# Kernel tuning notes

Measured on AMD Instinct MI355X. Metric: run time of the kernel, lower is better.

## Reference

```python
import jax, jax.numpy as jnp
import numpy as np

N, E, FN, FE, HID, G, OUT = 50000, 1600000, 16, 8, 64, 8, 1
NEG_ATT = 0.2   # GATv2 attention LeakyReLU slope (PyG default)
NEG_ACT = 0.01  # F.leaky_relu / nn.LeakyReLU default slope
EPS_BN = 1e-5


def _lin(k, fi, fo):
    return jax.random.normal(k, (fi, fo), jnp.float32) / float(np.sqrt(fi))


def setup_inputs() -> dict:
    key = jax.random.key(0)
    ks = iter(jax.random.split(key, 64))
    nk = lambda: next(ks)
    d = {}
    d['x'] = jax.random.normal(nk(), (N, FN), jnp.float32)
    d['edge_index'] = jax.random.randint(nk(), (2, E), 0, N)
    d['edge_attr'] = jax.random.normal(nk(), (E, FE), jnp.float32)
    d['batch'] = jnp.sort(jax.random.randint(nk(), (N,), 0, G))
    d['node_W'] = _lin(nk(), FN, HID); d['node_b'] = jnp.zeros((HID,), jnp.float32)
    d['eemb_W'] = _lin(nk(), FE, HID); d['eemb_b'] = jnp.zeros((HID,), jnp.float32)
    for i, h in enumerate((4, 4, 1)):
        c = HID // h
        d[f'Wl{i}'] = _lin(nk(), HID, HID); d[f'bl{i}'] = jnp.zeros((HID,), jnp.float32)
        d[f'Wr{i}'] = _lin(nk(), HID, HID); d[f'br{i}'] = jnp.zeros((HID,), jnp.float32)
        d[f'Wed{i}'] = _lin(nk(), HID, HID)  # lin_edge has bias=False in PyG
        d[f'att{i}'] = jax.random.normal(nk(), (h, c), jnp.float32) / float(np.sqrt(c))
        d[f'cb{i}'] = jnp.zeros((HID,), jnp.float32)
        d[f'g{i}'] = jnp.ones((HID,), jnp.float32); d[f'bt{i}'] = jnp.zeros((HID,), jnp.float32)
    d['ro1_W'] = _lin(nk(), HID, HID // 2); d['ro1_b'] = jnp.zeros((HID // 2,), jnp.float32)
    d['ro2_W'] = _lin(nk(), HID // 2, OUT); d['ro2_b'] = jnp.zeros((OUT,), jnp.float32)
    return d


def _gatv2(xn, src, dst, ea, Wl, bl, Wr, br, Wed, att, cb):
    # PyG GATv2Conv (concat=True, share_weights=False), self-loops already in src/dst/ea.
    n = xn.shape[0]
    h, c = att.shape
    xl = (xn @ Wl + bl).reshape(n, h, c)   # source transform (messages)
    xr = (xn @ Wr + br).reshape(n, h, c)   # destination transform
    e = (ea @ Wed).reshape(-1, h, c)       # edge transform
    m = jax.nn.leaky_relu(xl[src] + xr[dst] + e, NEG_ATT)  # [Etot,h,c]
    alpha = jnp.einsum('ehc,hc->eh', m, att)               # [Etot,h]
    amax = jax.lax.stop_gradient(jax.ops.segment_max(alpha, dst, num_segments=n))
    ex = jnp.exp(alpha - amax[dst])
    den = jax.ops.segment_sum(ex, dst, num_segments=n)
    a = ex / den[dst]                                      # segment softmax over in-edges
    out = jax.ops.segment_sum(a[:, :, None] * xl[src], dst, num_segments=n)
    return out.reshape(n, h * c) + cb


def _bn(x, g, b):
    # BatchNorm with batch statistics (training-mode normalization)
    mu = x.mean(0)
    var = x.var(0)
    return (x - mu) * jax.lax.rsqrt(var + EPS_BN) * g + b


def _forward(x, edge_index, edge_attr, batch, node_W, node_b, eemb_W, eemb_b,
             Wl0, bl0, Wr0, br0, Wed0, att0, cb0, g0, bt0,
             Wl1, bl1, Wr1, br1, Wed1, att1, cb1, g1, bt1,
             Wl2, bl2, Wr2, br2, Wed2, att2, cb2, g2, bt2,
             ro1_W, ro1_b, ro2_W, ro2_b):
    n = x.shape[0]
    loop = jnp.arange(n)
    src = jnp.concatenate([edge_index[0], loop])  # add self loops (PyG default)
    dst = jnp.concatenate([edge_index[1], loop])
    ea = jax.nn.leaky_relu(edge_attr @ eemb_W + eemb_b, NEG_ACT)  # edge_emb
    ea = jnp.concatenate([ea, jnp.broadcast_to(ea.mean(0), (n, HID))], 0)  # fill_value='mean'
    xh = x @ node_W + node_b
    layers = ((Wl0, bl0, Wr0, br0, Wed0, att0, cb0, g0, bt0),
              (Wl1, bl1, Wr1, br1, Wed1, att1, cb1, g1, bt1),
              (Wl2, bl2, Wr2, br2, Wed2, att2, cb2, g2, bt2))
    for (Wl, bl, Wr, br, Wed, att, cb, g, b) in layers:
        xh = _gatv2(xh, src, dst, ea, Wl, bl, Wr, br, Wed, att, cb)
        xh = jax.nn.leaky_relu(_bn(xh, g, b), NEG_ACT)
    pooled = jax.ops.segment_sum(xh, batch, num_segments=G)  # global_add_pool
    hidr = jax.nn.leaky_relu(pooled @ ro1_W + ro1_b, NEG_ACT)
    return hidr @ ro2_W + ro2_b


def reference(x, edge_index, edge_attr, batch, node_W, node_b, eemb_W, eemb_b,
              Wl0, bl0, Wr0, br0, Wed0, att0, cb0, g0, bt0,
              Wl1, bl1, Wr1, br1, Wed1, att1, cb1, g1, bt1,
              Wl2, bl2, Wr2, br2, Wed2, att2, cb2, g2, bt2,
              ro1_W, ro1_b, ro2_W, ro2_b):
    return _forward(x, edge_index, edge_attr, batch, node_W, node_b, eemb_W, eemb_b,
                    Wl0, bl0, Wr0, br0, Wed0, att0, cb0, g0, bt0,
                    Wl1, bl1, Wr1, br1, Wed1, att1, cb1, g1, bt1,
                    Wl2, bl2, Wr2, br2, Wed2, att2, cb2, g2, bt2,
                    ro1_W, ro1_b, ro2_W, ro2_b)
```

## Files before the change

### kernel.cpp

```cpp
#include <hip/hip_runtime.h>
#include <stdint.h>

#define N_NODES 50000
#define N_EDGES 1600000
#define ETOT    (N_EDGES + N_NODES)
#define FN 16
#define FE 8
#define HID 64
#define NGR 8
#define NEG_ATT 0.2f
#define NEG_ACT 0.01f
#define EPS_BN 1e-5f
#define MEAN_BLOCKS 512
#define SELF_FLAG 0x40000000
#define SRC_MASK  0x3FFFFFFF
#define SCAN_BLOCKS 196

typedef __attribute__((ext_vector_type(8))) short short8;
typedef __attribute__((ext_vector_type(4))) float f32x4;

__device__ __forceinline__ float bf2f(unsigned short u) {
  union { unsigned int i; float f; } c; c.i = ((unsigned int)u) << 16; return c.f;
}
__device__ __forceinline__ unsigned short f2bf(float f) {
  union { float f; unsigned int i; } c; c.f = f;
  unsigned int r = c.i + 0x7FFFu + ((c.i >> 16) & 1u);
  return (unsigned short)(r >> 16);
}
__device__ __forceinline__ float lrelu(float x, float s) { return x > 0.f ? x : s * x; }

__global__ __launch_bounds__(256) void k_node_embed(
    const float* __restrict__ x, const float* __restrict__ W,
    const float* __restrict__ b, float* __restrict__ xh) {
  __shared__ float sW[FN * HID];
  int t = threadIdx.x;
  for (int i = t; i < FN * HID; i += 256) sW[i] = W[i];
  __syncthreads();
  int j = t & 63;
  int v = blockIdx.x * 4 + (t >> 6);
  const float* xr = x + v * FN;
  float acc = b[j];
#pragma unroll
  for (int k = 0; k < FN; ++k) acc += xr[k] * sW[k * HID + j];
  xh[v * HID + j] = acc;
}

__global__ __launch_bounds__(256) void k_hist(const int* __restrict__ ei,
                                              int* __restrict__ counts) {
  int i = blockIdx.x * blockDim.x + threadIdx.x;
  int stride = gridDim.x * blockDim.x;
  for (; i < N_EDGES; i += stride) atomicAdd(&counts[ei[N_EDGES + i]], 1);
}

__global__ __launch_bounds__(256) void k_scanA(const int* __restrict__ counts,
                                               int* __restrict__ row_ptr,
                                               int* __restrict__ blocksum) {
  __shared__ int s[256];
  int t = threadIdx.x;
  int v = blockIdx.x * 256 + t;
  int val = (v < N_NODES) ? counts[v] + 1 : 0;
  s[t] = val; __syncthreads();
  for (int off = 1; off < 256; off <<= 1) {
    int add = (t >= off) ? s[t - off] : 0;
    __syncthreads();
    s[t] += add;
    __syncthreads();
  }
  if (v < N_NODES) row_ptr[v] = s[t] - val;
  if (t == 255) blocksum[blockIdx.x] = s[255];
}

__global__ __launch_bounds__(256) void k_scanB(const int* __restrict__ blocksum,
                                               int* __restrict__ blockoff,
                                               int* __restrict__ row_ptr) {
  __shared__ int s[256];
  int t = threadIdx.x;
  int val = (t < SCAN_BLOCKS) ? blocksum[t] : 0;
  s[t] = val; __syncthreads();
  for (int off = 1; off < 256; off <<= 1) {
    int add = (t >= off) ? s[t - off] : 0;
    __syncthreads();
    s[t] += add;
    __syncthreads();
  }
  if (t < SCAN_BLOCKS) blockoff[t] = s[t] - val;
  if (t == 255) row_ptr[N_NODES] = s[255];
}

__global__ __launch_bounds__(256) void k_scanC(int* __restrict__ row_ptr,
                                               int* __restrict__ fill,
                                               const int* __restrict__ blockoff) {
  int t = threadIdx.x;
  int v = blockIdx.x * 256 + t;
  if (v < N_NODES) {
    int rp = row_ptr[v] + blockoff[blockIdx.x];
    row_ptr[v] = rp;
    fill[v] = rp;
  }
}

__global__ __launch_bounds__(256) void k_scatter(const int* __restrict__ ei,
                                                 int* __restrict__ fill,
                                                 int2* __restrict__ srcperm) {
  int i = blockIdx.x * blockDim.x + threadIdx.x;
  int stride = gridDim.x * blockDim.x;
  for (; i < ETOT; i += stride) {
    if (i < N_EDGES) {
      int d = ei[N_EDGES + i];
      int pos = atomicAdd(&fill[d], 1);
      srcperm[pos] = make_int2(ei[i], i);
    } else {
      int v = i - N_EDGES;
      int pos = atomicAdd(&fill[v], 1);
      srcperm[pos] = make_int2(v | SELF_FLAG, 0);
    }
  }
}

__global__ __launch_bounds__(256) void k_attr_cvt(const float* __restrict__ eattr,
                                                  unsigned short* __restrict__ attr_bf) {
  int idx = blockIdx.x * 256 + threadIdx.x;
  float4 a = ((const float4*)eattr)[idx];
  unsigned int lo = (unsigned int)f2bf(a.x) | ((unsigned int)f2bf(a.y) << 16);
  unsigned int hi = (unsigned int)f2bf(a.z) | ((unsigned int)f2bf(a.w) << 16);
  ((int2*)attr_bf)[idx] = make_int2((int)lo, (int)hi);
}

__global__ __launch_bounds__(256) void k_meanp(const float* __restrict__ eattr,
                                               const float* __restrict__ eW,
                                               const float* __restrict__ eb,
                                               float* __restrict__ partial) {
  __shared__ float sA[256 * FE];
  __shared__ float sred[256];
  int t = threadIdx.x; int j = t & 63; int w = t >> 6;
  float Wj[8];
#pragma unroll
  for (int k = 0; k < 8; ++k) Wj[k] = eW[k * HID + j];
  float bj = eb[j], msum = 0.f;
  const int TILES = N_EDGES / 256;
  for (int tile = blockIdx.x; tile < TILES; tile += gridDim.x) {
    __syncthreads();
    const float4* src = (const float4*)(eattr + (size_t)tile * 256 * FE);
    ((float4*)sA)[t] = src[t];
    ((float4*)sA)[t + 256] = src[t + 256];
    __syncthreads();
#pragma unroll 8
    for (int e = 0; e < 64; ++e) {
      const float4* ar = (const float4*)(sA + (w * 64 + e) * FE);
      float4 A0 = ar[0], A1 = ar[1];
      float acc = bj + A0.x * Wj[0] + A0.y * Wj[1] + A0.z * Wj[2] + A0.w * Wj[3]
                     + A1.x * Wj[4] + A1.y * Wj[5] + A1.z * Wj[6] + A1.w * Wj[7];
      msum += lrelu(acc, NEG_ACT);
    }
  }
  sred[t] = msum; __syncthreads();
  if (w == 0)
    partial[blockIdx.x * HID + j] = sred[j] + sred[j + 64] + sred[j + 128] + sred[j + 192];
}

__global__ __launch_bounds__(256) void k_mean(const float* __restrict__ partial,
                                              float* __restrict__ mean) {
  __shared__ float sred[256];
  int t = threadIdx.x; int j = t & 63; int w = t >> 6;
  float s = 0.f;
  for (int bk = w; bk < MEAN_BLOCKS; bk += 4) s += partial[bk * HID + j];
  sred[t] = s; __syncthreads();
  if (w == 0)
    mean[j] = (sred[j] + sred[j + 64] + sred[j + 128] + sred[j + 192]) / (float)N_EDGES;
}

__global__ void k_eself(const float* __restrict__ meanv,
                        const float* __restrict__ Wed,
                        float* __restrict__ e_self) {
  int j = threadIdx.x;
  float s = 0.f;
  for (int k = 0; k < HID; ++k) s += meanv[k] * Wed[k * HID + j];
  e_self[j] = s;
}

__global__ __launch_bounds__(256) void k_xlr(const float* __restrict__ xh,
                                             const float* __restrict__ Wl,
                                             const float* __restrict__ bl,
                                             const float* __restrict__ Wr,
                                             const float* __restrict__ br,
                                             unsigned short* __restrict__ xl_bf,
                                             float* __restrict__ xr) {
  __shared__ float sWl[HID * HID], sWr[HID * HID];
  __shared__ float srow[4][HID];
  int t = threadIdx.x;
  for (int i = t; i < HID * HID; i += 256) { sWl[i] = Wl[i]; sWr[i] = Wr[i]; }
  __syncthreads();
  int j = t & 63; int w = t >> 6;
  int v = blockIdx.x * 4 + w;
  srow[w][j] = xh[v * HID + j];
  __syncthreads();
  float accL = bl[j], accR = br[j];
#pragma unroll
  for (int k = 0; k < HID; ++k) {
    float xk = srow[w][k];
    accL += xk * sWl[k * HID + j];
    accR += xk * sWr[k * HID + j];
  }
  xl_bf[v * HID + j] = f2bf(accL);
  xr[v * HID + j] = accR;
}

template <int HW>
__global__ __launch_bounds__(256) void k_attn_f(
    const unsigned short* __restrict__ xl_bf, const float* __restrict__ xr,
    const unsigned short* __restrict__ attr_bf,
    const int2* __restrict__ srcperm, const int* __restrict__ row_ptr,
    const float* __restrict__ eW, const float* __restrict__ eb,
    const float* __restrict__ Wed, const float* __restrict__ e_self,
    const float* __restrict__ att, const float* __restrict__ cb,
    float* __restrict__ xo) {
  __shared__ __align__(16) char smem[9216 + 16896];
  unsigned short* T1   = (unsigned short*)smem;
  unsigned short* sWed = (unsigned short*)(smem + 9216);
  unsigned short* sEw  = (unsigned short*)(smem + 9216 + 8192);
  float*          sEb  = (float*)(smem + 9216 + 8192 + 1024);
  float*          T2   = (float*)(smem + 9216);

  int t = threadIdx.x;
  for (int i = t; i < HID * HID; i += 256) sWed[i] = f2bf(Wed[i]);
  for (int i = t; i < FE * HID; i += 256) sEw[i] = f2bf(eW[i]);
  if (t < HID) sEb[t] = eb[t];
  __syncthreads();

  int lane = t & 63, w = t >> 6, l15 = lane & 15, lg = lane >> 4;

  short8 bW[4][2];
#pragma unroll
  for (int jc = 0; jc < 4; ++jc)
#pragma unroll
    for (int kh = 0; kh < 2; ++kh)
#pragma unroll
      for (int i = 0; i < 8; ++i)
        bW[jc][kh][i] = (short)sWed[(8 * lg + i + 32 * kh) * HID + jc * 16 + l15];
  short8 bE[4] = {};
  if (lg == 0)
#pragma unroll
    for (int jc = 0; jc < 4; ++jc)
#pragma unroll
      for (int i = 0; i < 8; ++i)
        bE[jc][i] = (short)sEw[i * HID + jc * 16 + l15];
  float biasv[4];
#pragma unroll
  for (int jc = 0; jc < 4; ++jc) biasv[jc] = sEb[jc * 16 + l15];
  __syncthreads();

  int v = blockIdx.x * 4 + w;
  if (v >= N_NODES) return;

  float xrv = xr[v * HID + lane];
  float attj = att[lane];
  float esj = e_self[lane];
  float cbj = cb[lane];
  int beg = row_ptr[v], end = row_ptr[v + 1];
  float M = -3.0e38f, S = 0.f, acc = 0.f;

  unsigned short* T1w = T1 + w * 16 * 72;
  float* T2w = T2 + w * 16 * 66;

  for (int base = beg; base < end; base += 16) {
    int cnt = end - base; if (cnt > 16) cnt = 16;
    int eidx = base + l15; if (eidx >= end) eidx = end - 1;
    int2 sp = srcperm[eidx];

    float xls[16];
#pragma unroll
    for (int i = 0; i < 16; ++i) {
      int raw = __builtin_amdgcn_readlane(sp.x, i);
      unsigned srcv = (unsigned)(raw & SRC_MASK);
      xls[i] = bf2f(xl_bf[srcv * 64u + (unsigned)lane]);
    }

    short8 a0 = {};
    if (lg == 0 && !(sp.x & SELF_FLAG))
      a0 = *(const short8*)(attr_bf + (size_t)sp.y * FE);
    f32x4 accE[4];
#pragma unroll
    for (int jc = 0; jc < 4; ++jc) {
      f32x4 z = {};
      accE[jc] = __builtin_amdgcn_mfma_f32_16x16x32_bf16(a0, bE[jc], z, 0, 0, 0);
    }
#pragma unroll
    for (int jc = 0; jc < 4; ++jc)
#pragma unroll
      for (int i = 0; i < 4; ++i)
        T1w[(4 * lg + i) * 72 + jc * 16 + l15] =
            f2bf(lrelu(accE[jc][i] + biasv[jc], NEG_ACT));
    __builtin_amdgcn_wave_barrier();
    asm volatile("s_waitcnt lgkmcnt(0)" ::: "memory");
    __builtin_amdgcn_sched_barrier(0);

    short8 A0 = *(const short8*)&T1w[l15 * 72 + 8 * lg];
    short8 A1 = *(const short8*)&T1w[l15 * 72 + 32 + 8 * lg];
    f32x4 acc2[4];
#pragma unroll
    for (int jc = 0; jc < 4; ++jc) {
      f32x4 z = {};
      acc2[jc] = __builtin_amdgcn_mfma_f32_16x16x32_bf16(A0, bW[jc][0], z, 0, 0, 0);
      acc2[jc] = __builtin_amdgcn_mfma_f32_16x16x32_bf16(A1, bW[jc][1], acc2[jc], 0, 0, 0);
    }
#pragma unroll
    for (int jc = 0; jc < 4; ++jc)
#pragma unroll
      for (int i = 0; i < 4; ++i)
        T2w[(4 * lg + i) * 66 + jc * 16 + l15] = acc2[jc][i];
    __builtin_amdgcn_wave_barrier();
    asm volatile("s_waitcnt lgkmcnt(0)" ::: "memory");
    __builtin_amdgcn_sched_barrier(0);

    float r[16];
#pragma unroll
    for (int i = 0; i < 16; ++i) {
      int raw = __builtin_amdgcn_readlane(sp.x, i);
      float e = (raw & SELF_FLAG) ? esj : T2w[i * 66 + lane];
      float mm = lrelu(xls[i] + xrv + e, NEG_ATT) * attj;
#pragma unroll
      for (int o = 1; o < HW; o <<= 1) mm += __shfl_xor(mm, o, 64);
      r[i] = (i < cnt) ? mm : -3.0e38f;
    }
    float mx = r[0];
#pragma unroll
    for (int i = 1; i < 16; ++i) mx = fmaxf(mx, r[i]);
    float Mn = fmaxf(M, mx);
    float sc = __expf(M - Mn);
    acc *= sc; S *= sc;
#pragma unroll
    for (int i = 0; i < 16; ++i) {
      float wi = __expf(r[i] - Mn);
      S += wi;
      acc += wi * xls[i];
    }
    M = Mn;
    __builtin_amdgcn_wave_barrier();
  }
  xo[v * HID + lane] = acc / S + cbj;
}

__global__ __launch_bounds__(256) void k_bnstats(const float* __restrict__ xo,
                                                 float* __restrict__ bns) {
  __shared__ float s1[256], s2[256];
  int t = threadIdx.x; int j = t & 63; int r = t >> 6;
  float sum = 0.f, sq = 0.f;
  int stride = gridDim.x * 4;
  for (int v = blockIdx.x * 4 + r; v < N_NODES; v += stride) {
    float x = xo[v * HID + j];
    sum += x; sq += x * x;
  }
  s1[t] = sum; s2[t] = sq; __syncthreads();
  if (r == 0) {
    atomicAdd(&bns[j], s1[j] + s1[j + 64] + s1[j + 128] + s1[j + 192]);
    atomicAdd(&bns[64 + j], s2[j] + s2[j + 64] + s2[j + 128] + s2[j + 192]);
  }
}

__global__ __launch_bounds__(256) void k_bnapply(const float* __restrict__ xo,
                                                 const float* __restrict__ bns,
                                                 const float* __restrict__ g,
                                                 const float* __restrict__ b,
                                                 float* __restrict__ xh) {
  int tid = blockIdx.x * 256 + threadIdx.x;
  int j = tid & 63;
  int v = tid >> 6;
  if (v >= N_NODES) return;
  const float invN = 1.f / (float)N_NODES;
  float mu = bns[j] * invN;
  float var = bns[64 + j] * invN - mu * mu;
  var = fmaxf(var, 0.f);
  float y = (xo[v * HID + j] - mu) * rsqrtf(var + EPS_BN) * g[j] + b[j];
  xh[v * HID + j] = lrelu(y, NEG_ACT);
}

__global__ __launch_bounds__(256) void k_pool(const float* __restrict__ xh,
                                              const int* __restrict__ batch,
                                              float* __restrict__ pooled) {
  __shared__ float lacc[4][NGR][HID];
  int t = threadIdx.x; int j = t & 63; int r = t >> 6;
  float a[NGR];
#pragma unroll
  for (int gg = 0; gg < NGR; ++gg) a[gg] = 0.f;
  int stride = gridDim.x * 4;
  for (int v = blockIdx.x * 4 + r; v < N_NODES; v += stride) {
    int g = batch[v];
    float x = xh[v * HID + j];
#pragma unroll
    for (int gg = 0; gg < NGR; ++gg) a[gg] += (g == gg) ? x : 0.f;
  }
#pragma unroll
  for (int gg = 0; gg < NGR; ++gg) lacc[r][gg][j] = a[gg];
  __syncthreads();
  if (r == 0) {
#pragma unroll
    for (int gg = 0; gg < NGR; ++gg)
      atomicAdd(&pooled[gg * HID + j],
                lacc[0][gg][j] + lacc[1][gg][j] + lacc[2][gg][j] + lacc[3][gg][j]);
  }
}

__global__ __launch_bounds__(256) void k_readout(const float* __restrict__ pooled,
                                                 const float* __restrict__ W1,
                                                 const float* __restrict__ b1,
                                                 const float* __restrict__ W2,
                                                 const float* __restrict__ b2,
                                                 float* __restrict__ out) {
  __shared__ float hid[NGR][32];
  int t = threadIdx.x;
  int g = t >> 5, q = t & 31;
  float acc = b1[q];
  for (int k = 0; k < HID; ++k) acc += pooled[g * HID + k] * W1[k * 32 + q];
  hid[g][q] = lrelu(acc, NEG_ACT);
  __syncthreads();
  if (t < NGR) {
    float o = b2[0];
    for (int q2 = 0; q2 < 32; ++q2) o += hid[t][q2] * W2[q2];
    out[t] = o;
  }
}

extern "C" void kernel_launch(void* const* d_in, const int* in_sizes, int n_in,
                              void* d_out, int out_size, void* d_ws, size_t ws_size,
                              hipStream_t stream) {
  (void)in_sizes; (void)n_in; (void)out_size; (void)ws_size;
  const float* x      = (const float*)d_in[0];
  const int*   ei     = (const int*)d_in[1];
  const float* eattr  = (const float*)d_in[2];
  const int*   batch  = (const int*)d_in[3];
  const float* node_W = (const float*)d_in[4];
  const float* node_b = (const float*)d_in[5];
  const float* eemb_W = (const float*)d_in[6];
  const float* eemb_b = (const float*)d_in[7];
  const float* ro1_W  = (const float*)d_in[35];
  const float* ro1_b  = (const float*)d_in[36];
  const float* ro2_W  = (const float*)d_in[37];
  const float* ro2_b  = (const float*)d_in[38];
  float* out = (float*)d_out;

  char* p = (char*)d_ws;
  auto alloc = [&](size_t bytes) {
    char* r = p;
    p += (bytes + 255) & ~(size_t)255;
    return r;
  };
  int*   counts = (int*)alloc((size_t)N_NODES * 4);
  float* bns    = (float*)alloc(3 * 128 * 4);
  float* pooled = (float*)alloc(NGR * HID * 4);
  size_t zero_bytes = (size_t)(p - (char*)d_ws);
  int*   row_ptr  = (int*)alloc((size_t)(N_NODES + 1) * 4);
  int*   fill     = (int*)alloc((size_t)N_NODES * 4);
  int*   blocksum = (int*)alloc((size_t)SCAN_BLOCKS * 4);
  int*   blockoff = (int*)alloc((size_t)SCAN_BLOCKS * 4);
  int2*  srcperm  = (int2*)alloc((size_t)ETOT * 8);
  unsigned short* attr_bf = (unsigned short*)alloc((size_t)N_EDGES * FE * 2);
  float* partial = (float*)alloc((size_t)MEAN_BLOCKS * HID * 4);
  float* meanv   = (float*)alloc(HID * 4);
  float* e_self  = (float*)alloc(HID * 4);
  float* xh      = (float*)alloc((size_t)N_NODES * HID * 4);
  unsigned short* xl_bf = (unsigned short*)alloc((size_t)N_NODES * HID * 2);
  float* xr      = (float*)alloc((size_t)N_NODES * HID * 4);
  float* xo      = xh;

  hipMemsetAsync(d_ws, 0, zero_bytes, stream);

  k_node_embed<<<N_NODES / 4, 256, 0, stream>>>(x, node_W, node_b, xh);
  k_hist<<<1024, 256, 0, stream>>>(ei, counts);
  k_scanA<<<SCAN_BLOCKS, 256, 0, stream>>>(counts, row_ptr, blocksum);
  k_scanB<<<1, 256, 0, stream>>>(blocksum, blockoff, row_ptr);
  k_scanC<<<SCAN_BLOCKS, 256, 0, stream>>>(row_ptr, fill, blockoff);
  k_scatter<<<1024, 256, 0, stream>>>(ei, fill, srcperm);
  k_attr_cvt<<<N_EDGES * FE / 4 / 256, 256, 0, stream>>>(eattr, attr_bf);
  k_meanp<<<MEAN_BLOCKS, 256, 0, stream>>>(eattr, eemb_W, eemb_b, partial);
  k_mean<<<1, 256, 0, stream>>>(partial, meanv);

  const int ablocks = (N_NODES + 3) / 4;
  for (int L = 0; L < 3; ++L) {
    const float* Wl  = (const float*)d_in[8 + 9 * L + 0];
    const float* bl  = (const float*)d_in[8 + 9 * L + 1];
    const float* Wr  = (const float*)d_in[8 + 9 * L + 2];
    const float* br  = (const float*)d_in[8 + 9 * L + 3];
    const float* Wed = (const float*)d_in[8 + 9 * L + 4];
    const float* att = (const float*)d_in[8 + 9 * L + 5];
    const float* cb  = (const float*)d_in[8 + 9 * L + 6];
    const float* g   = (const float*)d_in[8 + 9 * L + 7];
    const float* bt  = (const float*)d_in[8 + 9 * L + 8];
    k_xlr<<<N_NODES / 4, 256, 0, stream>>>(xh, Wl, bl, Wr, br, xl_bf, xr);
    k_eself<<<1, 64, 0, stream>>>(meanv, Wed, e_self);
    if (L < 2)
      k_attn_f<16><<<ablocks, 256, 0, stream>>>(xl_bf, xr, attr_bf, srcperm, row_ptr,
                                                eemb_W, eemb_b, Wed, e_self, att, cb, xo);
    else
      k_attn_f<64><<<ablocks, 256, 0, stream>>>(xl_bf, xr, attr_bf, srcperm, row_ptr,
                                                eemb_W, eemb_b, Wed, e_self, att, cb, xo);
    k_bnstats<<<256, 256, 0, stream>>>(xo, bns + L * 128);
    k_bnapply<<<N_NODES * HID / 256, 256, 0, stream>>>(xo, bns + L * 128, g, bt, xh);
  }

  k_pool<<<64, 256, 0, stream>>>(xh, batch, pooled);
  k_readout<<<1, 256, 0, stream>>>(pooled, ro1_W, ro1_b, ro2_W, ro2_b, out);
}
```

Baseline: 1.629 ms.

## Split fused GATv2 attention into edge-parallel score and node aggregation kernels

The per-node fused attention kernel is replaced by two kernels. An edge-tiled scoring kernel processes fixed 16-edge tiles across the whole CSR edge list: it gathers xl+xr as MFMA accumulators, folds the edge projection and the attention dot product into MFMA ops, and writes per-edge alpha values. A per-node aggregation kernel then does an online softmax over the stored alphas. A precomputed per-edge destination array replaces per-node tiling, which removes the padding waste on ragged neighbour lists and the per-lane shuffle reductions. The costs are an extra alpha buffer written and read per layer, redundant gathers of xl, and edge attributes converted from fp32 on every layer instead of once.

```diff
diff --git a/kernel.cpp b/kernel.cpp
--- a/kernel.cpp
+++ b/kernel.cpp
@@ -117,13 +117,13 @@
   }
 }
 
-__global__ __launch_bounds__(256) void k_attr_cvt(const float* __restrict__ eattr,
-                                                  unsigned short* __restrict__ attr_bf) {
-  int idx = blockIdx.x * 256 + threadIdx.x;
-  float4 a = ((const float4*)eattr)[idx];
-  unsigned int lo = (unsigned int)f2bf(a.x) | ((unsigned int)f2bf(a.y) << 16);
-  unsigned int hi = (unsigned int)f2bf(a.z) | ((unsigned int)f2bf(a.w) << 16);
-  ((int2*)attr_bf)[idx] = make_int2((int)lo, (int)hi);
+__global__ __launch_bounds__(256) void k_filldst(const int* __restrict__ row_ptr,
+                                                 int* __restrict__ dst_s) {
+  int t = threadIdx.x; int lane = t & 63; int w = t >> 6;
+  int v = blockIdx.x * 4 + w;
+  if (v >= N_NODES) return;
+  int beg = row_ptr[v], end = row_ptr[v + 1];
+  for (int p = beg + lane; p < end; p += 64) dst_s[p] = v;
 }
 
 __global__ __launch_bounds__(256) void k_meanp(const float* __restrict__ eattr,
@@ -169,15 +169,6 @@
     mean[j] = (sred[j] + sred[j + 64] + sred[j + 128] + sred[j + 192]) / (float)N_EDGES;
 }
 
-__global__ void k_eself(const float* __restrict__ meanv,
-                        const float* __restrict__ Wed,
-                        float* __restrict__ e_self) {
-  int j = threadIdx.x;
-  float s = 0.f;
-  for (int k = 0; k < HID; ++k) s += meanv[k] * Wed[k * HID + j];
-  e_self[j] = s;
-}
-
 __global__ __launch_bounds__(256) void k_xlr(const float* __restrict__ xh,
                                              const float* __restrict__ Wl,
                                              const float* __restrict__ bl,
@@ -206,25 +197,23 @@
 }
 
 template <int HW>
-__global__ __launch_bounds__(256) void k_attn_f(
+__global__ __launch_bounds__(256) void k_score(
     const unsigned short* __restrict__ xl_bf, const float* __restrict__ xr,
-    const unsigned short* __restrict__ attr_bf,
-    const int2* __restrict__ srcperm, const int* __restrict__ row_ptr,
+    const float* __restrict__ eattr,
+    const int2* __restrict__ srcperm, const int* __restrict__ dst_s,
     const float* __restrict__ eW, const float* __restrict__ eb,
-    const float* __restrict__ Wed, const float* __restrict__ e_self,
-    const float* __restrict__ att, const float* __restrict__ cb,
-    float* __restrict__ xo) {
-  __shared__ __align__(16) char smem[9216 + 16896];
-  unsigned short* T1   = (unsigned short*)smem;
-  unsigned short* sWed = (unsigned short*)(smem + 9216);
-  unsigned short* sEw  = (unsigned short*)(smem + 9216 + 8192);
-  float*          sEb  = (float*)(smem + 9216 + 8192 + 1024);
-  float*          T2   = (float*)(smem + 9216);
+    const float* __restrict__ Wed, const float* __restrict__ meanv,
+    const float* __restrict__ att, float* __restrict__ alpha) {
+  __shared__ __align__(16) char smem[9728];
+  unsigned short* sWed = (unsigned short*)smem;
+  unsigned short* sEw  = (unsigned short*)(smem + 8192);
+  float* sEb  = (float*)(smem + 9216);
+  float* sMean= (float*)(smem + 9472);
 
   int t = threadIdx.x;
   for (int i = t; i < HID * HID; i += 256) sWed[i] = f2bf(Wed[i]);
   for (int i = t; i < FE * HID; i += 256) sEw[i] = f2bf(eW[i]);
-  if (t < HID) sEb[t] = eb[t];
+  if (t < HID) { sEb[t] = eb[t]; sMean[t] = meanv[t]; }
   __syncthreads();
 
   int lane = t & 63, w = t >> 6, l15 = lane & 15, lg = lane >> 4;
@@ -245,99 +234,159 @@
       for (int i = 0; i < 8; ++i)
         bE[jc][i] = (short)sEw[i * HID + jc * 16 + l15];
   float biasv[4];
-#pragma unroll
-  for (int jc = 0; jc < 4; ++jc) biasv[jc] = sEb[jc * 16 + l15];
-  __syncthreads();
-
+  unsigned short meanbf[4];
+#pragma unroll
+  for (int jc = 0; jc < 4; ++jc) {
+    biasv[jc] = sEb[jc * 16 + l15];
+    meanbf[jc] = f2bf(sMean[jc * 16 + l15]);
+  }
+  short8 bH[2];
+#pragma unroll
+  for (int kh = 0; kh < 2; ++kh)
+#pragma unroll
+    for (int i = 0; i < 8; ++i) {
+      int k = 8 * lg + i + 32 * kh;
+      int hd = (HW == 16) ? (k >> 4) : 0;
+      bH[kh][i] = (hd == l15) ? (short)f2bf(att[k]) : (short)0;
+    }
+  __syncthreads();
+
+  unsigned short* T = (unsigned short*)(smem + w * 2304);
+
+  const int TILES = ETOT / 16;
+  int stride = gridDim.x * 4;
+  for (int tile = blockIdx.x * 4 + w; tile < TILES; tile += stride) {
+    int base = tile * 16;
+    int2 rl = srcperm[base + l15];
+    int4 rA = *(const int4*)(srcperm + base + 4 * lg);
+    int4 rB = *(const int4*)(srcperm + base + 4 * lg + 2);
+    int4 d4 = *(const int4*)(dst_s + base + 4 * lg);
+    int recx[4] = {rA.x, rA.z, rB.x, rB.z};
+    int dstv[4] = {d4.x, d4.y, d4.z, d4.w};
+
+    f32x4 c2[4];
+#pragma unroll
+    for (int jc = 0; jc < 4; ++jc)
+#pragma unroll
+      for (int i = 0; i < 4; ++i) {
+        unsigned s = (unsigned)(recx[i] & SRC_MASK);
+        c2[jc][i] = bf2f(xl_bf[(size_t)s * HID + jc * 16 + l15]) +
+                    xr[(size_t)dstv[i] * HID + jc * 16 + l15];
+      }
+
+    short8 a0 = {};
+    if (lg == 0 && !(rl.x & SELF_FLAG)) {
+      const float4* ap = (const float4*)(eattr + (size_t)rl.y * FE);
+      float4 A0 = ap[0], A1 = ap[1];
+      a0[0] = (short)f2bf(A0.x); a0[1] = (short)f2bf(A0.y);
+      a0[2] = (short)f2bf(A0.z); a0[3] = (short)f2bf(A0.w);
+      a0[4] = (short)f2bf(A1.x); a0[5] = (short)f2bf(A1.y);
+      a0[6] = (short)f2bf(A1.z); a0[7] = (short)f2bf(A1.w);
+    }
+    f32x4 accE[4];
+#pragma unroll
+    for (int jc = 0; jc < 4; ++jc) {
+      f32x4 z = {};
+      accE[jc] = __builtin_amdgcn_mfma_f32_16x16x32_bf16(a0, bE[jc], z, 0, 0, 0);
+    }
+#pragma unroll
+    for (int jc = 0; jc < 4; ++jc)
+#pragma unroll
+      for (int i = 0; i < 4; ++i) {
+        unsigned short val = (recx[i] & SELF_FLAG)
+            ? meanbf[jc]
+            : f2bf(lrelu(accE[jc][i] + biasv[jc], NEG_ACT));
+        T[(4 * lg + i) * 72 + jc * 16 + l15] = val;
+      }
+    __builtin_amdgcn_wave_barrier();
+    asm volatile("s_waitcnt lgkmcnt(0)" ::: "memory");
+    __builtin_amdgcn_sched_barrier(0);
+
+    short8 A0 = *(const short8*)&T[l15 * 72 + 8 * lg];
+    short8 A1 = *(const short8*)&T[l15 * 72 + 32 + 8 * lg];
+    asm volatile("s_waitcnt lgkmcnt(0)" ::: "memory");
+    __builtin_amdgcn_sched_barrier(0);
+
+    f32x4 m2[4];
+#pragma unroll
+    for (int jc = 0; jc < 4; ++jc) {
+      m2[jc] = __builtin_amdgcn_mfma_f32_16x16x32_bf16(A0, bW[jc][0], c2[jc], 0, 0, 0);
+      m2[jc] = __builtin_amdgcn_mfma_f32_16x16x32_bf16(A1, bW[jc][1], m2[jc], 0, 0, 0);
+    }
+#pragma unroll
+    for (int jc = 0; jc < 4; ++jc)
+#pragma unroll
+      for (int i = 0; i < 4; ++i)
+        T[(4 * lg + i) * 72 + jc * 16 + l15] = f2bf(lrelu(m2[jc][i], NEG_ATT));
+    __builtin_amdgcn_wave_barrier();
+    asm volatile("s_waitcnt lgkmcnt(0)" ::: "memory");
+    __builtin_amdgcn_sched_barrier(0);
+
+    short8 A30 = *(const short8*)&T[l15 * 72 + 8 * lg];
+    short8 A31 = *(const short8*)&T[l15 * 72 + 32 + 8 * lg];
+    asm volatile("s_waitcnt lgkmcnt(0)" ::: "memory");
+    __builtin_amdgcn_sched_barrier(0);
+
+    f32x4 r3 = {};
+    r3 = __builtin_amdgcn_mfma_f32_16x16x32_bf16(A30, bH[0], r3, 0, 0, 0);
+    r3 = __builtin_amdgcn_mfma_f32_16x16x32_bf16(A31, bH[1], r3, 0, 0, 0);
+
+    if (HW == 16) {
+      if (l15 < 4) {
+#pragma unroll
+        for (int i = 0; i < 4; ++i)
+          alpha[(size_t)(base + 4 * lg + i) * 4 + l15] = r3[i];
+      }
+    } else {
+      if (l15 == 0) {
+#pragma unroll
+        for (int i = 0; i < 4; ++i)
+          alpha[(size_t)(base + 4 * lg + i) * 4] = r3[i];
+      }
+    }
+  }
+}
+
+template <int HW>
+__global__ __launch_bounds__(256) void k_aggr(
+    const unsigned short* __restrict__ xl_bf, const float* __restrict__ alpha,
+    const int2* __restrict__ srcperm, const int* __restrict__ row_ptr,
+    const float* __restrict__ cb, float* __restrict__ xo) {
+  int t = threadIdx.x, lane = t & 63, w = t >> 6, l15 = lane & 15;
   int v = blockIdx.x * 4 + w;
   if (v >= N_NODES) return;
-
-  float xrv = xr[v * HID + lane];
-  float attj = att[lane];
-  float esj = e_self[lane];
+  int head = (HW == 16) ? (lane >> 4) : 0;
   float cbj = cb[lane];
   int beg = row_ptr[v], end = row_ptr[v + 1];
   float M = -3.0e38f, S = 0.f, acc = 0.f;
 
-  unsigned short* T1w = T1 + w * 16 * 72;
-  float* T2w = T2 + w * 16 * 66;
-
   for (int base = beg; base < end; base += 16) {
     int cnt = end - base; if (cnt > 16) cnt = 16;
     int eidx = base + l15; if (eidx >= end) eidx = end - 1;
-    int2 sp = srcperm[eidx];
-
-    float xls[16];
-#pragma unroll
-    for (int i = 0; i < 16; ++i) {
-      int raw = __builtin_amdgcn_readlane(sp.x, i);
-      unsigned srcv = (unsigned)(raw & SRC_MASK);
-      xls[i] = bf2f(xl_bf[srcv * 64u + (unsigned)lane]);
-    }
-
-    short8 a0 = {};
-    if (lg == 0 && !(sp.x & SELF_FLAG))
-      a0 = *(const short8*)(attr_bf + (size_t)sp.y * FE);
-    f32x4 accE[4];
-#pragma unroll
-    for (int jc = 0; jc < 4; ++jc) {
-      f32x4 z = {};
-      accE[jc] = __builtin_amdgcn_mfma_f32_16x16x32_bf16(a0, bE[jc], z, 0, 0, 0);
-    }
-#pragma unroll
-    for (int jc = 0; jc < 4; ++jc)
-#pragma unroll
-      for (int i = 0; i < 4; ++i)
-        T1w[(4 * lg + i) * 72 + jc * 16 + l15] =
-            f2bf(lrelu(accE[jc][i] + biasv[jc], NEG_ACT));
-    __builtin_amdgcn_wave_barrier();
-    asm volatile("s_waitcnt lgkmcnt(0)" ::: "memory");
-    __builtin_amdgcn_sched_barrier(0);
-
-    short8 A0 = *(const short8*)&T1w[l15 * 72 + 8 * lg];
-    short8 A1 = *(const short8*)&T1w[l15 * 72 + 32 + 8 * lg];
-    f32x4 acc2[4];
-#pragma unroll
-    for (int jc = 0; jc < 4; ++jc) {
-      f32x4 z = {};
-      acc2[jc] = __builtin_amdgcn_mfma_f32_16x16x32_bf16(A0, bW[jc][0], z, 0, 0, 0);
-      acc2[jc] = __builtin_amdgcn_mfma_f32_16x16x32_bf16(A1, bW[jc][1], acc2[jc], 0, 0, 0);
-    }
-#pragma unroll
-    for (int jc = 0; jc < 4; ++jc)
-#pragma unroll
-      for (int i = 0; i < 4; ++i)
-        T2w[(4 * lg + i) * 66 + jc * 16 + l15] = acc2[jc][i];
-    __builtin_amdgcn_wave_barrier();
-    asm volatile("s_waitcnt lgkmcnt(0)" ::: "memory");
-    __builtin_amdgcn_sched_barrier(0);
-
-    float r[16];
-#pragma unroll
-    for (int i = 0; i < 16; ++i) {
-      int raw = __builtin_amdgcn_readlane(sp.x, i);
-      float e = (raw & SELF_FLAG) ? esj : T2w[i * 66 + lane];
-      float mm = lrelu(xls[i] + xrv + e, NEG_ATT) * attj;
-#pragma unroll
-      for (int o = 1; o < HW; o <<= 1) mm += __shfl_xor(mm, o, 64);
-      r[i] = (i < cnt) ? mm : -3.0e38f;
-    }
-    float mx = r[0];
-#pragma unroll
-    for (int i = 1; i < 16; ++i) mx = fmaxf(mx, r[i]);
-    float Mn = fmaxf(M, mx);
-    float sc = __expf(M - Mn);
-    acc *= sc; S *= sc;
-#pragma unroll
-    for (int i = 0; i < 16; ++i) {
-      float wi = __expf(r[i] - Mn);
-      S += wi;
-      acc += wi * xls[i];
-    }
-    M = Mn;
-    __builtin_amdgcn_wave_barrier();
-  }
-  xo[v * HID + lane] = acc / S + cbj;
+    int spx = srcperm[eidx].x;
+#define AGLOAD(j, idx) { \
+      int raw = __builtin_amdgcn_readlane(spx, (idx)); \
+      unsigned s = (unsigned)(raw & SRC_MASK); \
+      xls_[j] = bf2f(xl_bf[(size_t)s * HID + lane]); \
+      float av = alpha[(size_t)(base + (idx)) * 4 + head]; \
+      a_[j] = ((idx) < cnt) ? av : -3.0e38f; }
+#define AGROUP(G) if (cnt > 4 * (G)) { \
+      float a_[4], xls_[4]; \
+      AGLOAD(0, 4*(G)) AGLOAD(1, 4*(G)+1) AGLOAD(2, 4*(G)+2) AGLOAD(3, 4*(G)+3) \
+      float mx = fmaxf(fmaxf(a_[0], a_[1]), fmaxf(a_[2], a_[3])); \
+      float Mn = fmaxf(M, mx); \
+      float sc = __expf(M - Mn); \
+      acc *= sc; S *= sc; \
+      { float wg = __expf(a_[0] - Mn); S += wg; acc += wg * xls_[0]; } \
+      { float wg = __expf(a_[1] - Mn); S += wg; acc += wg * xls_[1]; } \
+      { float wg = __expf(a_[2] - Mn); S += wg; acc += wg * xls_[2]; } \
+      { float wg = __expf(a_[3] - Mn); S += wg; acc += wg * xls_[3]; } \
+      M = Mn; }
+    AGROUP(0) AGROUP(1) AGROUP(2) AGROUP(3)
+#undef AGROUP
+#undef AGLOAD
+  }
+  xo[(size_t)v * HID + lane] = acc / S + cbj;
 }
 
 __global__ __launch_bounds__(256) void k_bnstats(const float* __restrict__ xo,
@@ -453,14 +502,14 @@
   int*   blocksum = (int*)alloc((size_t)SCAN_BLOCKS * 4);
   int*   blockoff = (int*)alloc((size_t)SCAN_BLOCKS * 4);
   int2*  srcperm  = (int2*)alloc((size_t)ETOT * 8);
-  unsigned short* attr_bf = (unsigned short*)alloc((size_t)N_EDGES * FE * 2);
-  float* partial = (float*)alloc((size_t)MEAN_BLOCKS * HID * 4);
-  float* meanv   = (float*)alloc(HID * 4);
-  float* e_self  = (float*)alloc(HID * 4);
-  float* xh      = (float*)alloc((size_t)N_NODES * HID * 4);
+  int*   dst_s    = (int*)alloc((size_t)ETOT * 4);
+  float* partial  = (float*)alloc((size_t)MEAN_BLOCKS * HID * 4);
+  float* meanv    = (float*)alloc(HID * 4);
+  float* alpha    = (float*)alloc(((size_t)ETOT + 16) * 4 * 4);
+  float* xh       = (float*)alloc((size_t)N_NODES * HID * 4);
   unsigned short* xl_bf = (unsigned short*)alloc((size_t)N_NODES * HID * 2);
-  float* xr      = (float*)alloc((size_t)N_NODES * HID * 4);
-  float* xo      = xh;
+  float* xr       = (float*)alloc((size_t)N_NODES * HID * 4);
+  float* xo       = xh;
 
   hipMemsetAsync(d_ws, 0, zero_bytes, stream);
 
@@ -470,7 +519,7 @@
   k_scanB<<<1, 256, 0, stream>>>(blocksum, blockoff, row_ptr);
   k_scanC<<<SCAN_BLOCKS, 256, 0, stream>>>(row_ptr, fill, blockoff);
   k_scatter<<<1024, 256, 0, stream>>>(ei, fill, srcperm);
-  k_attr_cvt<<<N_EDGES * FE / 4 / 256, 256, 0, stream>>>(eattr, attr_bf);
+  k_filldst<<<(N_NODES + 3) / 4, 256, 0, stream>>>(row_ptr, dst_s);
   k_meanp<<<MEAN_BLOCKS, 256, 0, stream>>>(eattr, eemb_W, eemb_b, partial);
   k_mean<<<1, 256, 0, stream>>>(partial, meanv);
 
@@ -486,13 +535,15 @@
     const float* g   = (const float*)d_in[8 + 9 * L + 7];
     const float* bt  = (const float*)d_in[8 + 9 * L + 8];
     k_xlr<<<N_NODES / 4, 256, 0, stream>>>(xh, Wl, bl, Wr, br, xl_bf, xr);
-    k_eself<<<1, 64, 0, stream>>>(meanv, Wed, e_self);
-    if (L < 2)
-      k_attn_f<16><<<ablocks, 256, 0, stream>>>(xl_bf, xr, attr_bf, srcperm, row_ptr,
-                                                eemb_W, eemb_b, Wed, e_self, att, cb, xo);
-    else
-      k_attn_f<64><<<ablocks, 256, 0, stream>>>(xl_bf, xr, attr_bf, srcperm, row_ptr,
-                                                eemb_W, eemb_b, Wed, e_self, att, cb, xo);
+    if (L < 2) {
+      k_score<16><<<1024, 256, 0, stream>>>(xl_bf, xr, eattr, srcperm, dst_s,
+                                            eemb_W, eemb_b, Wed, meanv, att, alpha);
+      k_aggr<16><<<ablocks, 256, 0, stream>>>(xl_bf, alpha, srcperm, row_ptr, cb, xo);
+    } else {
+      k_score<64><<<1024, 256, 0, stream>>>(xl_bf, xr, eattr, srcperm, dst_s,
+                                            eemb_W, eemb_b, Wed, meanv, att, alpha);
+      k_aggr<64><<<ablocks, 256, 0, stream>>>(xl_bf, alpha, srcperm, row_ptr, cb, xo);
+    }
     k_bnstats<<<256, 256, 0, stream>>>(xo, bns + L * 128);
     k_bnapply<<<N_NODES * HID / 256, 256, 0, stream>>>(xo, bns + L * 128, g, bt, xh);
   }
```

Result: faster. 1.348 ms (-17.3%).
